# Kernel optimization log

Hardware: AMD Instinct MI355X
Metric: run time of the kernel (lower is better)

The kernel has to match this reference:

```python
import math
import jax, jax.numpy as jnp
import numpy as np

NUM_BINS = 8
TRANS = 8
LEFT, RIGHT = -1.0, 1.0
MIN_W = MIN_H = MIN_D = 1.0e-4


def setup_inputs() -> dict:
    key = jax.random.key(0)
    ks = jax.random.split(key, 8)
    B, D, H, OUT = 524288, 16, 256, TRANS * (3 * NUM_BINS - 1)
    x = jax.random.uniform(ks[0], (B, D), jnp.float32, -0.99, 0.99)
    W0 = jax.random.normal(ks[1], (8, H), jnp.float32) * (1.0 / math.sqrt(8))
    b0 = jnp.zeros((H,), jnp.float32)
    W1 = jax.random.normal(ks[2], (H, H), jnp.float32) * (1.0 / math.sqrt(H))
    b1 = jnp.zeros((H,), jnp.float32)
    Wout = jax.random.normal(ks[3], (H, OUT), jnp.float32) * (0.1 / math.sqrt(H))
    bout = jnp.zeros((OUT,), jnp.float32)
    return {"x": x, "W0": W0, "b0": b0, "W1": W1, "b1": b1, "Wout": Wout, "bout": bout}


def _rq_spline(x, raw_w, raw_h, raw_d):
    # x: [B, T]; raw_w/raw_h: [B, T, K]; raw_d: [B, T, K-1]
    span = RIGHT - LEFT
    const = math.log(math.exp(1.0 - MIN_D) - 1.0)
    widths = jax.nn.softmax(raw_w, axis=-1)
    heights = jax.nn.softmax(raw_h, axis=-1)
    derivs = jax.nn.softplus(raw_d + const) + MIN_D
    widths = span * (MIN_W + (1.0 - MIN_W * NUM_BINS) * widths)
    heights = span * (MIN_H + (1.0 - MIN_H * NUM_BINS) * heights)
    edge_x = LEFT + jnp.pad(jnp.cumsum(widths, axis=-1), ((0, 0), (0, 0), (1, 0)))
    edge_y = LEFT + jnp.pad(jnp.cumsum(heights, axis=-1), ((0, 0), (0, 0), (1, 0)))
    derivs = jnp.pad(derivs, ((0, 0), (0, 0), (1, 1)), constant_values=1.0)
    out_mask = (x <= LEFT + 1e-3) | (x >= RIGHT - 1e-3)
    x_in = jnp.where(out_mask, 0.0, x)
    # searchsorted(right=True) - 1 == count of edges <= x_in, minus 1
    idx = jnp.clip(jnp.sum(edge_x <= x_in[..., None], axis=-1) - 1, 0, NUM_BINS - 1)
    g = lambda a: jnp.take_along_axis(a, idx[..., None], axis=-1)[..., 0]
    xk, yk = g(edge_x), g(edge_y)
    wk, hk = g(widths), g(heights)
    dk, dk1 = g(derivs), g(derivs[..., 1:])
    sk = hk / wk
    eps = (x_in - xk) / wk
    eps_term = eps * (1.0 - eps)
    eps2 = eps * eps
    beta = sk + (dk1 + dk - 2.0 * sk) * eps_term
    alpha = hk * (sk * eps2 + dk * eps_term)
    output = jnp.where(out_mask, x, yk + alpha / beta)
    logdet = (2.0 * jnp.log(sk)
              + jnp.log(dk1 * eps2 + 2.0 * sk * eps_term + dk * (1.0 - eps) ** 2)
              - 2.0 * jnp.log(beta))
    logdet = jnp.where(out_mask, 0.0, logdet)
    return output, logdet


def reference(x, W0, b0, W1, b1, Wout, bout):
    x1 = x[..., :TRANS]   # transformed half (mask == True)
    x2 = x[..., TRANS:]   # conditioning half
    h = jax.nn.relu(x2 @ W0 + b0)
    h = jax.nn.relu(h @ W1 + b1)
    raw = (h @ Wout + bout).reshape(x.shape[0], TRANS, 3 * NUM_BINS - 1)
    raw_w = raw[..., :NUM_BINS]
    raw_h = raw[..., NUM_BINS:2 * NUM_BINS]
    raw_d = raw[..., 2 * NUM_BINS:]
    y1, logdet = _rq_spline(x1, raw_w, raw_h, raw_d)
    out = jnp.concatenate([y1, x2], axis=-1)
    return out, jnp.sum(logdet, axis=-1)
```

## Files before the change

kernel.cpp:

```cpp
#include <hip/hip_runtime.h>
#include <hip/hip_bf16.h>


typedef __bf16 bf16x8 __attribute__((ext_vector_type(8)));
typedef __bf16 bf16x4v __attribute__((ext_vector_type(4)));
typedef float  f32x8 __attribute__((ext_vector_type(8)));
typedef float  f32x4 __attribute__((ext_vector_type(4)));
typedef float  f32x2 __attribute__((ext_vector_type(2)));

#define MFMA16(a,b,c) __builtin_amdgcn_mfma_f32_16x16x32_bf16((a),(b),(c),0,0,0)

#define SW_W1_OFF 8192
#define SW_WO_OFF 73728
#define SW_TOTAL  122880

#define ROWS    64
#define HSTRIDE 264
#define LOG2E   1.44269504f
#define LN2     0.69314718f
#define SPCONST 0.7806568f
#define ZSENT  (-0.00015680f)

__global__ void prep_kernel(const float* __restrict__ W0,
                            const float* __restrict__ W1,
                            const float* __restrict__ Wout,
                            __bf16* __restrict__ sw)
{
  int i = blockIdx.x * 256 + threadIdx.x;
  if (i >= SW_TOTAL) return;
  const float* src; int K, N, NT, li;
  float scale = 1.0f;
  if (i < SW_W1_OFF)      { src = W0;   K = 8;   N = 256; NT = 16; li = i; }
  else if (i < SW_WO_OFF) { src = W1;   K = 256; N = 256; NT = 16; li = i - SW_W1_OFF; }
  else { src = Wout; K = 256; N = 184; NT = 12; li = i - SW_WO_OFF; scale = LOG2E; }
  int j    = li & 7;
  int l    = (li >> 3) & 63;
  int rest = li >> 9;
  int nt   = rest % NT;
  int kb   = rest / NT;
  int k = kb * 32 + ((l >> 4) << 3) + j;
  int n = nt * 16 + (l & 15);
  float v = (k < K && n < N) ? src[k * N + n] * scale : 0.0f;
  sw[i] = (__bf16)v;
}

__device__ __forceinline__ bf16x4v relu_cvt4(f32x4 acc, float4 bb){
  f32x4 s;
  s[0] = acc[0] + bb.x; s[1] = acc[1] + bb.y;
  s[2] = acc[2] + bb.z; s[3] = acc[3] + bb.w;
  f32x4 z = {0.f, 0.f, 0.f, 0.f};
  s = __builtin_elementwise_max(s, z);
  return __builtin_convertvector(s, bf16x4v);
}

__global__ __launch_bounds__(512, 4)
void fused_kernel(const float* __restrict__ x,
                  const float* __restrict__ b0v,
                  const float* __restrict__ b1v,
                  const float* __restrict__ boutv,
                  const __bf16* __restrict__ sw,
                  float* __restrict__ out,
                  int nrows)
{
  __shared__ __align__(16) unsigned char smem[ROWS * HSTRIDE * 2];
  __shared__ __align__(16) float ldet[512];
  __bf16* hbuf = (__bf16*)smem;
  __bf16* rawb = hbuf;

  const int tid  = threadIdx.x;
  const int wave = tid >> 6;
  const int lane = tid & 63;
  const int quad = lane >> 4;
  const int l16  = lane & 15;
  const int row0 = blockIdx.x * ROWS;

  const __bf16* swW1 = sw + SW_W1_OFF;
  const __bf16* swWo = sw + SW_WO_OFF;
  const f32x4 z4 = {0.f, 0.f, 0.f, 0.f};

  if (tid < 2*ROWS){
    int r = tid >> 1, hf = tid & 1;
    long g = (long)row0 + r;
    *(float4*)(out + g*16 + 8 + hf*4) = *(const float4*)(x + g*16 + 8 + hf*4);
  }

  const int mq = wave >> 1;
  const int nh = wave & 1;

  {
    bf16x8 bfr[2];
    #pragma unroll
    for (int nt = 0; nt < 2; nt++){
      bf16x8 b = {};
      if (quad == 0){
        const float* xp = x + (long)(row0 + (nh*2 + nt)*16 + l16)*16 + 8;
        float4 u = *(const float4*)xp;
        float4 v = *(const float4*)(xp + 4);
        f32x8 xf; xf[0]=u.x; xf[1]=u.y; xf[2]=u.z; xf[3]=u.w;
                  xf[4]=v.x; xf[5]=v.y; xf[6]=v.z; xf[7]=v.w;
        b = __builtin_convertvector(xf, bf16x8);
      }
      bfr[nt] = b;
    }
    #pragma unroll
    for (int mi = 0; mi < 4; mi++){
      int mt = mq*4 + mi;
      bf16x8 a = *(const bf16x8*)(sw + (mt*64 + lane)*8);
      f32x4 acc0 = MFMA16(a, bfr[0], z4);
      f32x4 acc1 = MFMA16(a, bfr[1], z4);
      float4 bb = *(const float4*)(b0v + mt*16 + quad*4);
      *(bf16x4v*)(hbuf + ((nh*2+0)*16 + l16)*HSTRIDE + mt*16 + quad*4) = relu_cvt4(acc0, bb);
      *(bf16x4v*)(hbuf + ((nh*2+1)*16 + l16)*HSTRIDE + mt*16 + quad*4) = relu_cvt4(acc1, bb);
    }
  }
  __syncthreads();

  {
    f32x4 acc[4][2];
    #pragma unroll
    for (int mi=0;mi<4;mi++){ acc[mi][0]=z4; acc[mi][1]=z4; }
    #pragma unroll
    for (int kb=0;kb<8;kb++){
      bf16x8 bfr[2];
      #pragma unroll
      for (int nt=0;nt<2;nt++)
        bfr[nt] = *(const bf16x8*)(hbuf + ((nh*2+nt)*16 + l16)*HSTRIDE + kb*32 + quad*8);
      #pragma unroll
      for (int mi=0;mi<4;mi++){
        bf16x8 a = *(const bf16x8*)(swW1 + ((kb*16 + mq*4 + mi)*64 + lane)*8);
        acc[mi][0] = MFMA16(a, bfr[0], acc[mi][0]);
        acc[mi][1] = MFMA16(a, bfr[1], acc[mi][1]);
      }
    }
    __syncthreads();
    #pragma unroll
    for (int mi=0;mi<4;mi++){
      int mt = mq*4 + mi;
      float4 bb = *(const float4*)(b1v + mt*16 + quad*4);
      #pragma unroll
      for (int nt=0;nt<2;nt++)
        *(bf16x4v*)(hbuf + ((nh*2+nt)*16 + l16)*HSTRIDE + mt*16 + quad*4) = relu_cvt4(acc[mi][nt], bb);
    }
  }
  __syncthreads();

  {
    const int mh = wave >> 2;
    const int nc = wave & 3;
    f32x4 acc[2][3];
    #pragma unroll
    for (int mi=0;mi<2;mi++)
      #pragma unroll
      for (int ni=0;ni<3;ni++) acc[mi][ni] = z4;
    #pragma unroll
    for (int kb=0;kb<8;kb++){
      bf16x8 af[2];
      #pragma unroll
      for (int mi=0;mi<2;mi++)
        af[mi] = *(const bf16x8*)(hbuf + ((mh*2+mi)*16 + l16)*HSTRIDE + kb*32 + quad*8);
      #pragma unroll
      for (int ni=0;ni<3;ni++){
        bf16x8 b = *(const bf16x8*)(swWo + ((kb*12 + nc*3 + ni)*64 + lane)*8);
        acc[0][ni] = MFMA16(af[0], b, acc[0][ni]);
        acc[1][ni] = MFMA16(af[1], b, acc[1][ni]);
      }
    }
    __syncthreads();
    #pragma unroll
    for (int ni=0;ni<3;ni++){
      int col = (nc*3 + ni)*16 + l16;
      if (col < 184){
        int t = (col * 713) >> 14;
        float bias = boutv[col] * LOG2E;
        #pragma unroll
        for (int mi=0;mi<2;mi++)
          #pragma unroll
          for (int r=0;r<4;r++){
            int row = (mh*2+mi)*16 + quad*4 + r;
            rawb[row*HSTRIDE + col + t] = (__bf16)(acc[mi][ni][r] + bias);
          }
      }
    }
  }
  __syncthreads();

  {
    int row = tid >> 3;
    int t   = tid & 7;
    long gr = row0 + row;
    float xv = x[gr*16 + t];

    const __bf16* rr = rawb + row*HSTRIDE + t*24;
    bf16x8 v0 = *(const bf16x8*)(rr);
    bf16x8 v1 = *(const bf16x8*)(rr + 8);
    bf16x8 v2 = *(const bf16x8*)(rr + 16);

    f32x2 ewh[8];
    f32x2 sum = {0.f, 0.f};
    #pragma unroll
    for (int i=0;i<8;i++){
      f32x2 e;
      e[0] = __builtin_amdgcn_exp2f((float)v0[i]);
      e[1] = __builtin_amdgcn_exp2f((float)v1[i]);
      ewh[i] = e; sum += e;
    }
    f32x2 scale;
    scale[0] = 1.9984f * __builtin_amdgcn_rcpf(sum[0]);
    scale[1] = 1.9984f * __builtin_amdgcn_rcpf(sum[1]);
    const f32x2 off2 = {2e-4f, 2e-4f};

    bool msk = (xv <= -0.999f) || (xv >= 0.999f);
    float xin = msk ? 0.f : xv;

    f32x2 whi = ewh[0]*scale + off2;
    f32x2 ec; ec[0] = -1.f + whi[0]; ec[1] = -1.f + whi[1];
    f32x2 xyk = {-1.f, -1.f};
    f32x2 whk = whi;
    float zk = ZSENT, zk1 = (float)v2[0];
    #pragma unroll
    for (int i=1;i<8;i++){
      whi = ewh[i]*scale + off2;
      bool le = (ec[0] <= xin);
      xyk = le ? ec : xyk;
      whk = le ? whi : whk;
      zk  = le ? (float)v2[i-1] : zk;
      zk1 = le ? ((i==7) ? ZSENT : (float)v2[i]) : zk1;
      ec += whi;
    }

    float za = zk + SPCONST, zb = zk1 + SPCONST;
    float dk  = (fmaxf(za,0.f) + __builtin_amdgcn_logf(1.f + __builtin_amdgcn_exp2f(-fabsf(za))))*LN2 + 1e-4f;
    float dk1 = (fmaxf(zb,0.f) + __builtin_amdgcn_logf(1.f + __builtin_amdgcn_exp2f(-fabsf(zb))))*LN2 + 1e-4f;

    float rwk = __builtin_amdgcn_rcpf(whk[0]);
    float sk  = whk[1] * rwk;
    float eps = (xin - xyk[0]) * rwk;
    float om  = 1.f - eps;
    float et  = eps * om;
    float e2  = eps * eps;
    float beta  = sk + (dk1 + dk - 2.f*sk) * et;
    float rb    = __builtin_amdgcn_rcpf(beta);
    float alpha = whk[1] * (sk*e2 + dk*et);
    float yv  = msk ? xv : (xyk[1] + alpha * rb);
    float num = dk1*e2 + 2.f*sk*et + dk*om*om;
    float ld  = msk ? 0.f : __builtin_amdgcn_logf(sk*sk*num*rb*rb) * LN2;

    out[gr*16 + t] = yv;
    ldet[tid] = ld;
  }
  __syncthreads();

  if (tid < ROWS){
    float s = 0.f;
    #pragma unroll
    for (int t=0;t<8;t++) s += ldet[tid*8 + t];
    out[(long)nrows*16 + row0 + tid] = s;
  }
}

extern "C" void kernel_launch(void* const* d_in, const int* in_sizes, int n_in,
                              void* d_out, int out_size, void* d_ws, size_t ws_size,
                              hipStream_t stream)
{
  const float* x    = (const float*)d_in[0];
  const float* W0   = (const float*)d_in[1];
  const float* b0   = (const float*)d_in[2];
  const float* W1   = (const float*)d_in[3];
  const float* b1   = (const float*)d_in[4];
  const float* Wout = (const float*)d_in[5];
  const float* bout = (const float*)d_in[6];
  float* out = (float*)d_out;
  __bf16* sw = (__bf16*)d_ws;

  int nrows = in_sizes[0] / 16;
  int ntiles = nrows / ROWS;

  prep_kernel<<<(SW_TOTAL + 255)/256, 256, 0, stream>>>(W0, W1, Wout, sw);
  fused_kernel<<<ntiles, 512, 0, stream>>>(x, b0, b1, bout, sw, out, nrows);
}
```

Before: 243.5 us.

## Double rows per block to reuse weight fragments and shuffle-reduce logdet

Each block now handles 128 rows instead of 64, so every weight fragment loaded from global memory feeds four MFMAs instead of two in all three GEMM layers. This halves weight-load traffic per row and halves the number of blocks. The spline epilogue now has each thread process two rows. The per-row logdet sum uses a wavefront xor-shuffle reduction, which drops the LDS buffer and one barrier. The cost is double the shared memory per block and more accumulator registers, which may lower occupancy under launch_bounds(512,4).

```diff
diff --git a/kernel.cpp b/kernel.cpp
--- a/kernel.cpp
+++ b/kernel.cpp
@@ -14,7 +14,7 @@
 #define SW_WO_OFF 73728
 #define SW_TOTAL  122880
 
-#define ROWS    64
+#define ROWS    128
 #define HSTRIDE 264
 #define LOG2E   1.44269504f
 #define LN2     0.69314718f
@@ -63,7 +63,6 @@
                   int nrows)
 {
   __shared__ __align__(16) unsigned char smem[ROWS * HSTRIDE * 2];
-  __shared__ __align__(16) float ldet[512];
   __bf16* hbuf = (__bf16*)smem;
   __bf16* rawb = hbuf;
 
@@ -88,12 +87,12 @@
   const int nh = wave & 1;
 
   {
-    bf16x8 bfr[2];
-    #pragma unroll
-    for (int nt = 0; nt < 2; nt++){
+    bf16x8 bfr[4];
+    #pragma unroll
+    for (int nt = 0; nt < 4; nt++){
       bf16x8 b = {};
       if (quad == 0){
-        const float* xp = x + (long)(row0 + (nh*2 + nt)*16 + l16)*16 + 8;
+        const float* xp = x + (long)(row0 + (nh*4 + nt)*16 + l16)*16 + 8;
         float4 u = *(const float4*)xp;
         float4 v = *(const float4*)(xp + 4);
         f32x8 xf; xf[0]=u.x; xf[1]=u.y; xf[2]=u.z; xf[3]=u.w;
@@ -106,30 +105,34 @@
     for (int mi = 0; mi < 4; mi++){
       int mt = mq*4 + mi;
       bf16x8 a = *(const bf16x8*)(sw + (mt*64 + lane)*8);
-      f32x4 acc0 = MFMA16(a, bfr[0], z4);
-      f32x4 acc1 = MFMA16(a, bfr[1], z4);
       float4 bb = *(const float4*)(b0v + mt*16 + quad*4);
-      *(bf16x4v*)(hbuf + ((nh*2+0)*16 + l16)*HSTRIDE + mt*16 + quad*4) = relu_cvt4(acc0, bb);
-      *(bf16x4v*)(hbuf + ((nh*2+1)*16 + l16)*HSTRIDE + mt*16 + quad*4) = relu_cvt4(acc1, bb);
+      #pragma unroll
+      for (int nt = 0; nt < 4; nt++){
+        f32x4 acc = MFMA16(a, bfr[nt], z4);
+        *(bf16x4v*)(hbuf + ((nh*4+nt)*16 + l16)*HSTRIDE + mt*16 + quad*4) = relu_cvt4(acc, bb);
+      }
     }
   }
   __syncthreads();
 
   {
-    f32x4 acc[4][2];
-    #pragma unroll
-    for (int mi=0;mi<4;mi++){ acc[mi][0]=z4; acc[mi][1]=z4; }
+    f32x4 acc[4][4];
+    #pragma unroll
+    for (int mi=0;mi<4;mi++)
+      #pragma unroll
+      for (int bt=0;bt<4;bt++) acc[mi][bt] = z4;
     #pragma unroll
     for (int kb=0;kb<8;kb++){
-      bf16x8 bfr[2];
-      #pragma unroll
-      for (int nt=0;nt<2;nt++)
-        bfr[nt] = *(const bf16x8*)(hbuf + ((nh*2+nt)*16 + l16)*HSTRIDE + kb*32 + quad*8);
+      bf16x8 hf[4];
+      #pragma unroll
+      for (int bt=0;bt<4;bt++)
+        hf[bt] = *(const bf16x8*)(hbuf + ((nh*4+bt)*16 + l16)*HSTRIDE + kb*32 + quad*8);
       #pragma unroll
       for (int mi=0;mi<4;mi++){
         bf16x8 a = *(const bf16x8*)(swW1 + ((kb*16 + mq*4 + mi)*64 + lane)*8);
-        acc[mi][0] = MFMA16(a, bfr[0], acc[mi][0]);
-        acc[mi][1] = MFMA16(a, bfr[1], acc[mi][1]);
+        #pragma unroll
+        for (int bt=0;bt<4;bt++)
+          acc[mi][bt] = MFMA16(a, hf[bt], acc[mi][bt]);
       }
     }
     __syncthreads();
@@ -138,31 +141,32 @@
       int mt = mq*4 + mi;
       float4 bb = *(const float4*)(b1v + mt*16 + quad*4);
       #pragma unroll
-      for (int nt=0;nt<2;nt++)
-        *(bf16x4v*)(hbuf + ((nh*2+nt)*16 + l16)*HSTRIDE + mt*16 + quad*4) = relu_cvt4(acc[mi][nt], bb);
+      for (int bt=0;bt<4;bt++)
+        *(bf16x4v*)(hbuf + ((nh*4+bt)*16 + l16)*HSTRIDE + mt*16 + quad*4) = relu_cvt4(acc[mi][bt], bb);
     }
   }
   __syncthreads();
 
   {
+    const int nc = wave & 3;
     const int mh = wave >> 2;
-    const int nc = wave & 3;
-    f32x4 acc[2][3];
-    #pragma unroll
-    for (int mi=0;mi<2;mi++)
-      #pragma unroll
-      for (int ni=0;ni<3;ni++) acc[mi][ni] = z4;
+    f32x4 acc[4][3];
+    #pragma unroll
+    for (int bt=0;bt<4;bt++)
+      #pragma unroll
+      for (int ni=0;ni<3;ni++) acc[bt][ni] = z4;
     #pragma unroll
     for (int kb=0;kb<8;kb++){
-      bf16x8 af[2];
-      #pragma unroll
-      for (int mi=0;mi<2;mi++)
-        af[mi] = *(const bf16x8*)(hbuf + ((mh*2+mi)*16 + l16)*HSTRIDE + kb*32 + quad*8);
+      bf16x8 hf[4];
+      #pragma unroll
+      for (int bt=0;bt<4;bt++)
+        hf[bt] = *(const bf16x8*)(hbuf + ((mh*4+bt)*16 + l16)*HSTRIDE + kb*32 + quad*8);
       #pragma unroll
       for (int ni=0;ni<3;ni++){
         bf16x8 b = *(const bf16x8*)(swWo + ((kb*12 + nc*3 + ni)*64 + lane)*8);
-        acc[0][ni] = MFMA16(af[0], b, acc[0][ni]);
-        acc[1][ni] = MFMA16(af[1], b, acc[1][ni]);
+        #pragma unroll
+        for (int bt=0;bt<4;bt++)
+          acc[bt][ni] = MFMA16(hf[bt], b, acc[bt][ni]);
       }
     }
     __syncthreads();
@@ -173,20 +177,23 @@
         int t = (col * 713) >> 14;
         float bias = boutv[col] * LOG2E;
         #pragma unroll
-        for (int mi=0;mi<2;mi++)
+        for (int bt=0;bt<4;bt++)
           #pragma unroll
           for (int r=0;r<4;r++){
-            int row = (mh*2+mi)*16 + quad*4 + r;
-            rawb[row*HSTRIDE + col + t] = (__bf16)(acc[mi][ni][r] + bias);
+            int row = (mh*4+bt)*16 + quad*4 + r;
+            rawb[row*HSTRIDE + col + t] = (__bf16)(acc[bt][ni][r] + bias);
           }
       }
     }
   }
   __syncthreads();
 
-  {
-    int row = tid >> 3;
-    int t   = tid & 7;
+  float ldv[2];
+  #pragma unroll
+  for (int pp = 0; pp < 2; pp++){
+    int p   = tid + pp*512;
+    int row = p >> 3;
+    int t   = p & 7;
     long gr = row0 + row;
     float xv = x[gr*16 + t];
 
@@ -246,15 +253,19 @@
     float ld  = msk ? 0.f : __builtin_amdgcn_logf(sk*sk*num*rb*rb) * LN2;
 
     out[gr*16 + t] = yv;
-    ldet[tid] = ld;
-  }
-  __syncthreads();
-
-  if (tid < ROWS){
-    float s = 0.f;
-    #pragma unroll
-    for (int t=0;t<8;t++) s += ldet[tid*8 + t];
-    out[(long)nrows*16 + row0 + tid] = s;
+    ldv[pp] = ld;
+  }
+
+  float s0 = ldv[0], s1 = ldv[1];
+  #pragma unroll
+  for (int m = 1; m < 8; m <<= 1){
+    s0 += __shfl_xor(s0, m);
+    s1 += __shfl_xor(s1, m);
+  }
+  if ((lane & 7) == 0){
+    int r = tid >> 3;
+    out[(long)nrows*16 + row0 + r]      = s0;
+    out[(long)nrows*16 + row0 + r + 64] = s1;
   }
 }
 
```

Result: faster. 227.4 us (-6.6%).
